# Optimization experiments

Hardware: AMD Instinct MI355X
Metric: run time of the kernel (lower is better)

## Reference

```python
import jax, jax.numpy as jnp
import numpy as np

N_NODES = 100000
IN_DIM = 64
EMBED_DIM = 128
EDGE_DIM = 32
N_EDGES = 1600000
ALPHA = 0.5


def _glorot(key, shape):
    fan_in, fan_out = shape[0], shape[1]
    lim = np.sqrt(6.0 / (fan_in + fan_out))
    return jax.random.uniform(key, shape, jnp.float32, -lim, lim)


def setup_inputs() -> dict:
    key = jax.random.key(0)
    ks = jax.random.split(key, 20)
    inp = {
        "x": jax.random.normal(ks[0], (N_NODES, IN_DIM), jnp.float32),
        "edge_index": jax.random.randint(ks[1], (2, N_EDGES), 0, N_NODES, jnp.int64),
        "edge_attr": jax.random.normal(ks[2], (N_EDGES, EDGE_DIM), jnp.float32),
        # conv_in (GINEConv) params: edge lin (edge_dim->in_dim), MLP (in->embed->embed)
        "We_in": _glorot(ks[3], (EDGE_DIM, IN_DIM)),
        "be_in": jnp.zeros((IN_DIM,), jnp.float32),
        "W1_in": _glorot(ks[4], (IN_DIM, EMBED_DIM)),
        "b1_in": jnp.zeros((EMBED_DIM,), jnp.float32),
        "W2_in": _glorot(ks[5], (EMBED_DIM, EMBED_DIM)),
        "b2_in": jnp.zeros((EMBED_DIM,), jnp.float32),
        # conv_out (deep-copied GINEConv, independent params)
        "We_out": _glorot(ks[6], (EDGE_DIM, IN_DIM)),
        "be_out": jnp.zeros((IN_DIM,), jnp.float32),
        "W1_out": _glorot(ks[7], (IN_DIM, EMBED_DIM)),
        "b1_out": jnp.zeros((EMBED_DIM,), jnp.float32),
        "W2_out": _glorot(ks[8], (EMBED_DIM, EMBED_DIM)),
        "b2_out": jnp.zeros((EMBED_DIM,), jnp.float32),
        # root linear (in_dim -> embed_dim)
        "Wr": _glorot(ks[9], (IN_DIM, EMBED_DIM)),
        "br": jnp.zeros((EMBED_DIM,), jnp.float32),
    }
    return inp


def _gine(x, src, dst, edge_attr, We, be, W1, b1, W2, b2):
    # GINEConv: out = MLP((1+eps)*x + sum_j relu(x_j + lin(e_ji))), eps=0
    e = edge_attr @ We + be                       # [E, in_dim]
    msg = jax.nn.relu(x[src] + e)                 # gather + add + relu
    agg = jax.ops.segment_sum(msg, dst, num_segments=x.shape[0])
    h = x + agg
    h = jax.nn.gelu(h @ W1 + b1, approximate=False) @ W2 + b2
    return h


def reference(x, edge_index, edge_attr,
              We_in, be_in, W1_in, b1_in, W2_in, b2_in,
              We_out, be_out, W1_out, b1_out, W2_out, b2_out,
              Wr, br):
    src, dst = edge_index[0], edge_index[1]
    # conv_in: messages flow src -> dst (aggregate at dst)
    h_in = _gine(x, src, dst, edge_attr, We_in, be_in, W1_in, b1_in, W2_in, b2_in)
    # conv_out: flipped edges, messages flow dst -> src (aggregate at src)
    h_out = _gine(x, dst, src, edge_attr, We_out, be_out, W1_out, b1_out, W2_out, b2_out)
    out = ALPHA * h_out + (1.0 - ALPHA) * h_in + (x @ Wr + br)
    return out
```

## Files before the change

### kernel.cpp

```cpp
#include <hip/hip_runtime.h>
#include <hip/hip_bf16.h>
#include <hip/hip_fp16.h>
#include <math.h>

#define N_NODES 100000
#define IN_DIM 64
#define EMBED_DIM 128
#define EDGE_DIM 32
#define N_EDGES 1600000

typedef __attribute__((ext_vector_type(8))) short bf16x8;
typedef __attribute__((ext_vector_type(4))) float f32x4;

__device__ __forceinline__ ushort f2bf(float f) {
    union { float f; uint i; } v; v.f = f;
    uint x = v.i;
    return (ushort)((x + 0x7fffu + ((x >> 16) & 1u)) >> 16);
}

__global__ __launch_bounds__(256) void cvt_x_kernel(
    const float* __restrict__ x, __half* __restrict__ xh)
{
    const int i = blockIdx.x * blockDim.x + threadIdx.x;
    if (i < N_NODES * IN_DIM / 4) {
        float4 v = ((const float4*)x)[i];
        ((__half2*)xh)[2 * i]     = __floats2half2_rn(v.x, v.y);
        ((__half2*)xh)[2 * i + 1] = __floats2half2_rn(v.z, v.w);
    }
}

__global__ __launch_bounds__(256) void edge_kernel(
    const __half* __restrict__ xh, const int* __restrict__ ei,
    const float* __restrict__ ea,
    const float* __restrict__ We_in, const float* __restrict__ be_in,
    const float* __restrict__ We_out, const float* __restrict__ be_out,
    __half* __restrict__ agg_in, __half* __restrict__ agg_out)
{
    const int lane = threadIdx.x & 63;
    const int r = lane & 15;
    const int h = lane >> 4;
    const int wave = threadIdx.x >> 6;

    bf16x8 bIn[4], bOut[4];
    float beI[4], beO[4];
#pragma unroll
    for (int t = 0; t < 4; ++t) {
        const int cp = ((t >> 1) << 5) + (r << 1) + (t & 1);
        const float* p1 = We_in  + (h * 8) * 64 + cp;
        const float* p2 = We_out + (h * 8) * 64 + cp;
        bf16x8 b1v, b2v;
#pragma unroll
        for (int j = 0; j < 8; ++j) {
            b1v[j] = (short)f2bf(p1[j * 64]);
            b2v[j] = (short)f2bf(p2[j * 64]);
        }
        bIn[t] = b1v; bOut[t] = b2v;
        beI[t] = be_in[cp];
        beO[t] = be_out[cp];
    }

    const int nGroups = N_EDGES / 16;
    const int stride = gridDim.x * 4;
    for (int g = blockIdx.x * 4 + wave; g < nGroups; g += stride) {
        const int e0 = g * 16;
        const float* ap = ea + (size_t)(e0 + r) * 32 + h * 8;
        float4 av0 = *(const float4*)ap;
        float4 av1 = *(const float4*)(ap + 4);
        bf16x8 a;
        a[0] = (short)f2bf(av0.x); a[1] = (short)f2bf(av0.y);
        a[2] = (short)f2bf(av0.z); a[3] = (short)f2bf(av0.w);
        a[4] = (short)f2bf(av1.x); a[5] = (short)f2bf(av1.y);
        a[6] = (short)f2bf(av1.z); a[7] = (short)f2bf(av1.w);

        f32x4 cIn[4], cOut[4];
#pragma unroll
        for (int t = 0; t < 4; ++t) {
            f32x4 z = {0.f, 0.f, 0.f, 0.f};
            cIn[t]  = __builtin_amdgcn_mfma_f32_16x16x32_bf16(a, bIn[t],  z, 0, 0, 0);
            cOut[t] = __builtin_amdgcn_mfma_f32_16x16x32_bf16(a, bOut[t], z, 0, 0, 0);
        }

        const int4 s4 = *(const int4*)(ei + e0 + h * 4);
        const int4 d4 = *(const int4*)(ei + N_EDGES + e0 + h * 4);
        const int ss[4] = {s4.x, s4.y, s4.z, s4.w};
        const int dd[4] = {d4.x, d4.y, d4.z, d4.w};

#pragma unroll
        for (int i = 0; i < 4; ++i) {
            const int s = ss[i];
            const int d = dd[i];
#pragma unroll
            for (int tp = 0; tp < 2; ++tp) {
                const int coff = 32 * tp + 2 * r;
                __half2 xs = *(const __half2*)(xh + (size_t)s * 64 + coff);
                float m0 = fmaxf(__low2float(xs)  + cIn[2 * tp][i]     + beI[2 * tp],     0.0f);
                float m1 = fmaxf(__high2float(xs) + cIn[2 * tp + 1][i] + beI[2 * tp + 1], 0.0f);
                if (m0 != 0.0f || m1 != 0.0f)
                    unsafeAtomicAdd((__half2*)(agg_in + (size_t)d * 64 + coff),
                                    __floats2half2_rn(m0, m1));
                __half2 xd = *(const __half2*)(xh + (size_t)d * 64 + coff);
                float n0 = fmaxf(__low2float(xd)  + cOut[2 * tp][i]     + beO[2 * tp],     0.0f);
                float n1 = fmaxf(__high2float(xd) + cOut[2 * tp + 1][i] + beO[2 * tp + 1], 0.0f);
                if (n0 != 0.0f || n1 != 0.0f)
                    unsafeAtomicAdd((__half2*)(agg_out + (size_t)s * 64 + coff),
                                    __floats2half2_rn(n0, n1));
            }
        }
    }
}

#define T_STRIDE 136

__device__ __forceinline__ void gine_mlp(
    const float* __restrict__ x, const __half* __restrict__ agg,
    const float* __restrict__ W1, const float* __restrict__ b1,
    const float* __restrict__ W2,
    int n0, int r, int h, ushort* Tw, f32x4 hAcc[8])
{
    bf16x8 a0[2];
#pragma unroll
    for (int half_ = 0; half_ < 2; ++half_) {
        const int kb = half_ * 32 + h * 8;
        const float*  xp = x   + (size_t)(n0 + r) * 64 + kb;
        const __half* gp = agg + (size_t)(n0 + r) * 64 + kb;
        float4 x0 = *(const float4*)xp;
        float4 x1 = *(const float4*)(xp + 4);
        __half2 g0 = *(const __half2*)(gp);
        __half2 g1 = *(const __half2*)(gp + 2);
        __half2 g2 = *(const __half2*)(gp + 4);
        __half2 g3 = *(const __half2*)(gp + 6);
        bf16x8 v;
        v[0] = (short)f2bf(x0.x + __low2float(g0));
        v[1] = (short)f2bf(x0.y + __high2float(g0));
        v[2] = (short)f2bf(x0.z + __low2float(g1));
        v[3] = (short)f2bf(x0.w + __high2float(g1));
        v[4] = (short)f2bf(x1.x + __low2float(g2));
        v[5] = (short)f2bf(x1.y + __high2float(g2));
        v[6] = (short)f2bf(x1.z + __low2float(g3));
        v[7] = (short)f2bf(x1.w + __high2float(g3));
        a0[half_] = v;
    }

    __threadfence_block();

#pragma unroll
    for (int t = 0; t < 8; ++t) {
        const float* w1p = W1 + (h * 8) * 128 + 16 * t + r;
        bf16x8 b0v, b1v;
#pragma unroll
        for (int j = 0; j < 8; ++j) {
            b0v[j] = (short)f2bf(w1p[j * 128]);
            b1v[j] = (short)f2bf(w1p[4096 + j * 128]);
        }
        f32x4 acc = {0.f, 0.f, 0.f, 0.f};
        acc = __builtin_amdgcn_mfma_f32_16x16x32_bf16(a0[0], b0v, acc, 0, 0, 0);
        acc = __builtin_amdgcn_mfma_f32_16x16x32_bf16(a0[1], b1v, acc, 0, 0, 0);
        float bias = b1[16 * t + r];
#pragma unroll
        for (int i = 0; i < 4; ++i) {
            float v = acc[i] + bias;
            float g = 0.5f * v * (1.0f + erff(v * 0.70710678118654752f));
            Tw[(h * 4 + i) * T_STRIDE + 16 * t + r] = f2bf(g);
        }
    }

    __threadfence_block();

    bf16x8 aT[4];
#pragma unroll
    for (int ks = 0; ks < 4; ++ks)
        aT[ks] = *(const bf16x8*)(Tw + r * T_STRIDE + ks * 32 + h * 8);
#pragma unroll
    for (int t = 0; t < 8; ++t) {
        const float* w2p = W2 + (h * 8) * 128 + 16 * t + r;
        f32x4 acc = {0.f, 0.f, 0.f, 0.f};
#pragma unroll
        for (int ks = 0; ks < 4; ++ks) {
            bf16x8 bv;
#pragma unroll
            for (int j = 0; j < 8; ++j) bv[j] = (short)f2bf(w2p[(ks * 32 + j) * 128]);
            acc = __builtin_amdgcn_mfma_f32_16x16x32_bf16(aT[ks], bv, acc, 0, 0, 0);
        }
        hAcc[t] = acc;
    }
}

__global__ __launch_bounds__(256) void node_kernel(
    const float* __restrict__ x,
    const __half* __restrict__ agg_in, const __half* __restrict__ agg_out,
    const float* __restrict__ W1_in, const float* __restrict__ b1_in,
    const float* __restrict__ W2_in, const float* __restrict__ b2_in,
    const float* __restrict__ W1_out, const float* __restrict__ b1_out,
    const float* __restrict__ W2_out, const float* __restrict__ b2_out,
    const float* __restrict__ Wr, const float* __restrict__ br,
    float* __restrict__ out)
{
    const int lane = threadIdx.x & 63;
    const int r = lane & 15;
    const int h = lane >> 4;
    const int wave = threadIdx.x >> 6;

    __shared__ __align__(16) ushort Tld[4][16 * T_STRIDE];
    ushort* Tw = &Tld[wave][0];

    const int g = blockIdx.x * 4 + wave;
    if (g >= N_NODES / 16) return;
    const int n0 = g * 16;

    f32x4 hIn[8], hOut[8];
    gine_mlp(x, agg_in,  W1_in,  b1_in,  W2_in,  n0, r, h, Tw, hIn);
    gine_mlp(x, agg_out, W1_out, b1_out, W2_out, n0, r, h, Tw, hOut);

    bf16x8 ar[2];
#pragma unroll
    for (int half_ = 0; half_ < 2; ++half_) {
        const float* xp = x + (size_t)(n0 + r) * 64 + half_ * 32 + h * 8;
        bf16x8 v;
#pragma unroll
        for (int j = 0; j < 8; ++j) v[j] = (short)f2bf(xp[j]);
        ar[half_] = v;
    }

#pragma unroll
    for (int t = 0; t < 8; ++t) {
        const float* wrp = Wr + (h * 8) * 128 + 16 * t + r;
        bf16x8 b0v, b1v;
#pragma unroll
        for (int j = 0; j < 8; ++j) {
            b0v[j] = (short)f2bf(wrp[j * 128]);
            b1v[j] = (short)f2bf(wrp[4096 + j * 128]);
        }
        f32x4 rt = {0.f, 0.f, 0.f, 0.f};
        rt = __builtin_amdgcn_mfma_f32_16x16x32_bf16(ar[0], b0v, rt, 0, 0, 0);
        rt = __builtin_amdgcn_mfma_f32_16x16x32_bf16(ar[1], b1v, rt, 0, 0, 0);

        const int c = 16 * t + r;
        float b2i = b2_in[c];
        float b2o = b2_out[c];
        float brv = br[c];
#pragma unroll
        for (int i = 0; i < 4; ++i) {
            float o = 0.5f * (hOut[t][i] + b2o) + 0.5f * (hIn[t][i] + b2i) + rt[i] + brv;
            out[(size_t)(n0 + h * 4 + i) * 128 + c] = o;
        }
    }
}

extern "C" void kernel_launch(void* const* d_in, const int* in_sizes, int n_in,
                              void* d_out, int out_size, void* d_ws, size_t ws_size,
                              hipStream_t stream) {
    const float* x      = (const float*)d_in[0];
    const int*   ei     = (const int*)d_in[1];
    const float* ea     = (const float*)d_in[2];
    const float* We_in  = (const float*)d_in[3];
    const float* be_in  = (const float*)d_in[4];
    const float* W1_in  = (const float*)d_in[5];
    const float* b1_in  = (const float*)d_in[6];
    const float* W2_in  = (const float*)d_in[7];
    const float* b2_in  = (const float*)d_in[8];
    const float* We_out = (const float*)d_in[9];
    const float* be_out = (const float*)d_in[10];
    const float* W1_out = (const float*)d_in[11];
    const float* b1_out = (const float*)d_in[12];
    const float* W2_out = (const float*)d_in[13];
    const float* b2_out = (const float*)d_in[14];
    const float* Wr     = (const float*)d_in[15];
    const float* br     = (const float*)d_in[16];

    __half* agg_in  = (__half*)d_ws;
    __half* agg_out = agg_in + (size_t)N_NODES * IN_DIM;
    __half* x_h     = agg_out + (size_t)N_NODES * IN_DIM;
    const size_t agg_bytes = (size_t)2 * N_NODES * IN_DIM * sizeof(__half);

    hipMemsetAsync(d_ws, 0, agg_bytes, stream);

    cvt_x_kernel<<<(N_NODES * IN_DIM / 4 + 255) / 256, 256, 0, stream>>>(x, x_h);

    edge_kernel<<<2048, 256, 0, stream>>>(x_h, ei, ea, We_in, be_in, We_out, be_out,
                                          agg_in, agg_out);

    node_kernel<<<(N_NODES / 16 + 3) / 4, 256, 0, stream>>>(
        x, agg_in, agg_out,
        W1_in, b1_in, W2_in, b2_in,
        W1_out, b1_out, W2_out, b2_out,
        Wr, br, (float*)d_out);
}
```

Measured before the change: 499.7 us.

## Replace atomic scatter aggregation with CSR-sorted per-node gather aggregation

Builds per-direction CSR adjacency each call (degree histogram, scan, scatter into permutations) and replaces the half-precision atomic scatter-add edge kernel with a per-node gather kernel that accumulates messages in registers and writes fp32 aggregates once. Edge attributes are pre-converted to bf16 to halve gather traffic. This aims to remove the large volume of contended atomics, at the cost of extra preprocessing kernels, a serial scan, and gathering edge attributes twice. A fallback keeps the old path when the workspace is too small.

New measurement: 1.144 ms. 2.29x slower.

```diff
diff --git a/kernel.cpp b/kernel.cpp
--- a/kernel.cpp
+++ b/kernel.cpp
@@ -26,6 +26,173 @@
         float4 v = ((const float4*)x)[i];
         ((__half2*)xh)[2 * i]     = __floats2half2_rn(v.x, v.y);
         ((__half2*)xh)[2 * i + 1] = __floats2half2_rn(v.z, v.w);
+    }
+}
+
+__global__ __launch_bounds__(256) void cvt_ea_kernel(
+    const float* __restrict__ ea, ushort* __restrict__ eab)
+{
+    const int i = blockIdx.x * blockDim.x + threadIdx.x;
+    if (i < N_EDGES * EDGE_DIM / 4) {
+        float4 v = ((const float4*)ea)[i];
+        ushort4 o;
+        o.x = f2bf(v.x); o.y = f2bf(v.y); o.z = f2bf(v.z); o.w = f2bf(v.w);
+        ((ushort4*)eab)[i] = o;
+    }
+}
+
+__global__ __launch_bounds__(256) void hist_kernel(
+    const int* __restrict__ ei, int* __restrict__ deg_in, int* __restrict__ deg_out)
+{
+    const int e = blockIdx.x * blockDim.x + threadIdx.x;
+    if (e < N_EDGES) {
+        const int s = ei[e];
+        const int d = ei[N_EDGES + e];
+        atomicAdd(deg_in + d, 1);
+        atomicAdd(deg_out + s, 1);
+    }
+}
+
+__global__ __launch_bounds__(256) void scan_kernel(
+    const int* __restrict__ deg_in,  int* __restrict__ start_in,  int* __restrict__ pos_in,
+    const int* __restrict__ deg_out, int* __restrict__ start_out, int* __restrict__ pos_out)
+{
+    const int* deg = blockIdx.x ? deg_out : deg_in;
+    int* start     = blockIdx.x ? start_out : start_in;
+    int* pos       = blockIdx.x ? pos_out   : pos_in;
+    const int t = threadIdx.x;
+    const int C = (N_NODES + 255) / 256;
+    const int b0 = t * C;
+    int s = 0;
+    for (int k = 0; k < C; ++k) {
+        const int idx = b0 + k;
+        if (idx < N_NODES) s += deg[idx];
+    }
+    __shared__ int sc[256];
+    sc[t] = s;
+    __syncthreads();
+    for (int o = 1; o < 256; o <<= 1) {
+        const int v = (t >= o) ? sc[t - o] : 0;
+        __syncthreads();
+        sc[t] += v;
+        __syncthreads();
+    }
+    int ex = sc[t] - s;
+    for (int k = 0; k < C; ++k) {
+        const int idx = b0 + k;
+        if (idx < N_NODES) {
+            const int d = deg[idx];
+            start[idx] = ex;
+            pos[idx]   = ex;
+            ex += d;
+        }
+    }
+}
+
+__global__ __launch_bounds__(256) void scatter_kernel(
+    const int* __restrict__ ei,
+    int* __restrict__ pos_in, int* __restrict__ pos_out,
+    int2* __restrict__ perm_in, int2* __restrict__ perm_out)
+{
+    const int e = blockIdx.x * blockDim.x + threadIdx.x;
+    if (e < N_EDGES) {
+        const int s = ei[e];
+        const int d = ei[N_EDGES + e];
+        const int p = atomicAdd(pos_in + d, 1);
+        perm_in[p] = make_int2(e, s);
+        const int q = atomicAdd(pos_out + s, 1);
+        perm_out[q] = make_int2(e, d);
+    }
+}
+
+__global__ __launch_bounds__(256) void agg_kernel(
+    const __half* __restrict__ xh, const ushort* __restrict__ eab,
+    const float* __restrict__ We_in, const float* __restrict__ be_in,
+    const float* __restrict__ We_out, const float* __restrict__ be_out,
+    const int* __restrict__ start_in, const int* __restrict__ deg_in,
+    const int2* __restrict__ perm_in,
+    const int* __restrict__ start_out, const int* __restrict__ deg_out,
+    const int2* __restrict__ perm_out,
+    float* __restrict__ agg_in, float* __restrict__ agg_out)
+{
+    const int lane = threadIdx.x & 63;
+    const int r = lane & 15;
+    const int h = lane >> 4;
+    const int wave = threadIdx.x >> 6;
+
+    const bool dirOut = blockIdx.x >= 2048;
+    const float* We   = dirOut ? We_out : We_in;
+    const float* be   = dirOut ? be_out : be_in;
+    const int* start  = dirOut ? start_out : start_in;
+    const int* deg    = dirOut ? deg_out : deg_in;
+    const int2* perm  = dirOut ? perm_out : perm_in;
+    float* agg        = dirOut ? agg_out : agg_in;
+
+    bf16x8 bW[4];
+    float beV[4];
+#pragma unroll
+    for (int t = 0; t < 4; ++t) {
+        const int cp = ((t >> 1) << 5) + (r << 1) + (t & 1);
+        const float* p = We + (h * 8) * 64 + cp;
+        bf16x8 bv;
+#pragma unroll
+        for (int j = 0; j < 8; ++j) bv[j] = (short)f2bf(p[j * 64]);
+        bW[t] = bv;
+        beV[t] = be[cp];
+    }
+
+    const int wid = (blockIdx.x & 2047) * 4 + wave;
+    const int NPW = (N_NODES + 8191) / 8192;
+    const int n0 = wid * NPW;
+    const int n1 = min(N_NODES, n0 + NPW);
+
+    for (int n = n0; n < n1; ++n) {
+        const int st = start[n];
+        const int en = st + deg[n];
+        float accL[4] = {0.f, 0.f, 0.f, 0.f};
+
+        for (int c0 = st; c0 < en; c0 += 16) {
+            const int slot = c0 + r;
+            const int2 pe = perm[slot < en ? slot : en - 1];
+            const bf16x8 a = *(const bf16x8*)(eab + (size_t)pe.x * 32 + h * 8);
+
+            f32x4 C[4];
+#pragma unroll
+            for (int t = 0; t < 4; ++t) {
+                f32x4 z = {0.f, 0.f, 0.f, 0.f};
+                C[t] = __builtin_amdgcn_mfma_f32_16x16x32_bf16(a, bW[t], z, 0, 0, 0);
+            }
+
+            const int rem = en - c0;
+            const int ownOther = pe.y;
+#pragma unroll
+            for (int i = 0; i < 4; ++i) {
+                const int m = h * 4 + i;
+                const int other = __shfl(ownOther, m, 64);
+                const bool valid = m < rem;
+#pragma unroll
+                for (int tp = 0; tp < 2; ++tp) {
+                    const __half2 xs =
+                        *(const __half2*)(xh + (size_t)other * 64 + 32 * tp + 2 * r);
+                    float m0 = fmaxf(__low2float(xs)  + C[2 * tp][i]     + beV[2 * tp],     0.f);
+                    float m1 = fmaxf(__high2float(xs) + C[2 * tp + 1][i] + beV[2 * tp + 1], 0.f);
+                    if (valid) {
+                        accL[2 * tp]     += m0;
+                        accL[2 * tp + 1] += m1;
+                    }
+                }
+            }
+        }
+
+#pragma unroll
+        for (int t = 0; t < 4; ++t) {
+            accL[t] += __shfl_xor(accL[t], 16, 64);
+            accL[t] += __shfl_xor(accL[t], 32, 64);
+        }
+        if (h < 2) {
+            float2 v = make_float2(accL[2 * h], accL[2 * h + 1]);
+            *(float2*)(agg + (size_t)n * 64 + 32 * h + 2 * r) = v;
+        }
     }
 }
 
@@ -111,8 +278,24 @@
 
 #define T_STRIDE 136
 
+__device__ __forceinline__ void load8f(const float* __restrict__ p, float* o) {
+    float4 a = *(const float4*)p;
+    float4 b = *(const float4*)(p + 4);
+    o[0] = a.x; o[1] = a.y; o[2] = a.z; o[3] = a.w;
+    o[4] = b.x; o[5] = b.y; o[6] = b.z; o[7] = b.w;
+}
+__device__ __forceinline__ void load8f(const __half* __restrict__ p, float* o) {
+#pragma unroll
+    for (int j = 0; j < 4; ++j) {
+        __half2 g = *(const __half2*)(p + 2 * j);
+        o[2 * j]     = __low2float(g);
+        o[2 * j + 1] = __high2float(g);
+    }
+}
+
+template<typename AggT>
 __device__ __forceinline__ void gine_mlp(
-    const float* __restrict__ x, const __half* __restrict__ agg,
+    const float* __restrict__ x, const AggT* __restrict__ agg,
     const float* __restrict__ W1, const float* __restrict__ b1,
     const float* __restrict__ W2,
     int n0, int r, int h, ushort* Tw, f32x4 hAcc[8])
@@ -121,23 +304,12 @@
 #pragma unroll
     for (int half_ = 0; half_ < 2; ++half_) {
         const int kb = half_ * 32 + h * 8;
-        const float*  xp = x   + (size_t)(n0 + r) * 64 + kb;
-        const __half* gp = agg + (size_t)(n0 + r) * 64 + kb;
-        float4 x0 = *(const float4*)xp;
-        float4 x1 = *(const float4*)(xp + 4);
-        __half2 g0 = *(const __half2*)(gp);
-        __half2 g1 = *(const __half2*)(gp + 2);
-        __half2 g2 = *(const __half2*)(gp + 4);
-        __half2 g3 = *(const __half2*)(gp + 6);
+        float xv[8], gv[8];
+        load8f(x   + (size_t)(n0 + r) * 64 + kb, xv);
+        load8f(agg + (size_t)(n0 + r) * 64 + kb, gv);
         bf16x8 v;
-        v[0] = (short)f2bf(x0.x + __low2float(g0));
-        v[1] = (short)f2bf(x0.y + __high2float(g0));
-        v[2] = (short)f2bf(x0.z + __low2float(g1));
-        v[3] = (short)f2bf(x0.w + __high2float(g1));
-        v[4] = (short)f2bf(x1.x + __low2float(g2));
-        v[5] = (short)f2bf(x1.y + __high2float(g2));
-        v[6] = (short)f2bf(x1.z + __low2float(g3));
-        v[7] = (short)f2bf(x1.w + __high2float(g3));
+#pragma unroll
+        for (int j = 0; j < 8; ++j) v[j] = (short)f2bf(xv[j] + gv[j]);
         a0[half_] = v;
     }
 
@@ -185,9 +357,10 @@
     }
 }
 
+template<typename AggT>
 __global__ __launch_bounds__(256) void node_kernel(
     const float* __restrict__ x,
-    const __half* __restrict__ agg_in, const __half* __restrict__ agg_out,
+    const AggT* __restrict__ agg_in, const AggT* __restrict__ agg_out,
     const float* __restrict__ W1_in, const float* __restrict__ b1_in,
     const float* __restrict__ W2_in, const float* __restrict__ b2_in,
     const float* __restrict__ W1_out, const float* __restrict__ b1_out,
@@ -267,21 +440,60 @@
     const float* Wr     = (const float*)d_in[15];
     const float* br     = (const float*)d_in[16];
 
-    __half* agg_in  = (__half*)d_ws;
-    __half* agg_out = agg_in + (size_t)N_NODES * IN_DIM;
-    __half* x_h     = agg_out + (size_t)N_NODES * IN_DIM;
-    const size_t agg_bytes = (size_t)2 * N_NODES * IN_DIM * sizeof(__half);
-
-    hipMemsetAsync(d_ws, 0, agg_bytes, stream);
-
-    cvt_x_kernel<<<(N_NODES * IN_DIM / 4 + 255) / 256, 256, 0, stream>>>(x, x_h);
-
-    edge_kernel<<<2048, 256, 0, stream>>>(x_h, ei, ea, We_in, be_in, We_out, be_out,
-                                          agg_in, agg_out);
-
-    node_kernel<<<(N_NODES / 16 + 3) / 4, 256, 0, stream>>>(
-        x, agg_in, agg_out,
-        W1_in, b1_in, W2_in, b2_in,
-        W1_out, b1_out, W2_out, b2_out,
-        Wr, br, (float*)d_out);
-}
+    const size_t EAB_B   = (size_t)N_EDGES * EDGE_DIM * 2;
+    const size_t XH_B    = (size_t)N_NODES * IN_DIM * 2;
+    const size_t AGG_B   = (size_t)N_NODES * IN_DIM * 4;
+    const size_t PERM_B  = (size_t)N_EDGES * 8;
+    const size_t META_B  = (size_t)N_NODES * 4;
+    const size_t NEED    = EAB_B + XH_B + 2 * AGG_B + 2 * PERM_B + 6 * META_B;
+
+    if (ws_size >= NEED) {
+        char* w = (char*)d_ws;
+        ushort* eab     = (ushort*)w;                    w += EAB_B;
+        __half* xh      = (__half*)w;                    w += XH_B;
+        float* agg_in   = (float*)w;                     w += AGG_B;
+        float* agg_out  = (float*)w;                     w += AGG_B;
+        int2* perm_in   = (int2*)w;                      w += PERM_B;
+        int2* perm_out  = (int2*)w;                      w += PERM_B;
+        int* deg_in     = (int*)w;                       w += META_B;
+        int* deg_out    = (int*)w;                       w += META_B;
+        int* start_in   = (int*)w;                       w += META_B;
+        int* start_out  = (int*)w;                       w += META_B;
+        int* pos_in     = (int*)w;                       w += META_B;
+        int* pos_out    = (int*)w;
+
+        hipMemsetAsync(deg_in, 0, 2 * META_B, stream);
+
+        cvt_x_kernel<<<(N_NODES * IN_DIM / 4 + 255) / 256, 256, 0, stream>>>(x, xh);
+        cvt_ea_kernel<<<(N_EDGES * EDGE_DIM / 4 + 255) / 256, 256, 0, stream>>>(ea, eab);
+        hist_kernel<<<(N_EDGES + 255) / 256, 256, 0, stream>>>(ei, deg_in, deg_out);
+        scan_kernel<<<2, 256, 0, stream>>>(deg_in, start_in, pos_in,
+                                           deg_out, start_out, pos_out);
+        scatter_kernel<<<(N_EDGES + 255) / 256, 256, 0, stream>>>(
+            ei, pos_in, pos_out, perm_in, perm_out);
+        agg_kernel<<<4096, 256, 0, stream>>>(
+            xh, eab, We_in, be_in, We_out, be_out,
+            start_in, deg_in, perm_in, start_out, deg_out, perm_out,
+            agg_in, agg_out);
+        node_kernel<float><<<(N_NODES / 16 + 3) / 4, 256, 0, stream>>>(
+            x, agg_in, agg_out,
+            W1_in, b1_in, W2_in, b2_in,
+            W1_out, b1_out, W2_out, b2_out,
+            Wr, br, (float*)d_out);
+    } else {
+        __half* agg_in  = (__half*)d_ws;
+        __half* agg_out = agg_in + (size_t)N_NODES * IN_DIM;
+        __half* xh      = agg_out + (size_t)N_NODES * IN_DIM;
+        const size_t agg_bytes = (size_t)2 * N_NODES * IN_DIM * sizeof(__half);
+
+        hipMemsetAsync(d_ws, 0, agg_bytes, stream);
+        cvt_x_kernel<<<(N_NODES * IN_DIM / 4 + 255) / 256, 256, 0, stream>>>(x, xh);
+        edge_kernel<<<2048, 256, 0, stream>>>(xh, ei, ea, We_in, be_in, We_out, be_out,
+                                              agg_in, agg_out);
+        node_kernel<__half><<<(N_NODES / 16 + 3) / 4, 256, 0, stream>>>(
+            x, agg_in, agg_out,
+            W1_in, b1_in, W2_in, b2_in,
+            W1_out, b1_out, W2_out, b2_out,
+            Wr, br, (float*)d_out);
+    }
+}
```
